# Kernel tuning notes

Hardware: AMD Instinct MI355X
Metric: run time of the kernel (lower is better)

The kernel has to match this reference:

```python
import jax, jax.numpy as jnp
import numpy as np

EPS = 1e-8
THR = 1e-6


def setup_inputs() -> dict:
    key = jax.random.key(0)
    ks = jax.random.split(key, 16)
    B, N, E, F, H, NH = 2, 8192, 131072, 128, 256, 4
    D = H // NH          # per-head width = 64
    FEAT = 2 * F + 12    # 268 = 2F + radial + dist + dot + 9 so3
    s = 0.05
    return {
        "h": jax.random.normal(ks[0], (B, N, F), jnp.float32),
        "coord": jax.random.normal(ks[1], (B, N, 3), jnp.float32),
        "edge_index": jax.random.randint(ks[2], (2, E), 0, N),
        "edge_w1": jax.random.normal(ks[3], (NH, FEAT, D), jnp.float32) * s,
        "edge_b1": jnp.zeros((NH, D), jnp.float32),
        "edge_w2": jax.random.normal(ks[4], (NH, D, D), jnp.float32) * s,
        "edge_b2": jnp.zeros((NH, D), jnp.float32),
        "ln_g": jnp.ones((H,), jnp.float32),
        "ln_b": jnp.zeros((H,), jnp.float32),
        "node_w1": jax.random.normal(ks[5], (H + F, H), jnp.float32) * s,
        "node_b1": jnp.zeros((H,), jnp.float32),
        "node_w2": jax.random.normal(ks[6], (H, F), jnp.float32) * s,
        "node_b2": jnp.zeros((F,), jnp.float32),
        "coord_w1": jax.random.normal(ks[7], (H, H), jnp.float32) * s,
        "coord_b1": jnp.zeros((H,), jnp.float32),
        "coord_w2": jax.random.normal(ks[8], (H, 1), jnp.float32) * 0.001,  # xavier gain 0.001
    }


def reference(h, coord, edge_index, edge_w1, edge_b1, edge_w2, edge_b2,
              ln_g, ln_b, node_w1, node_b1, node_w2, node_b2,
              coord_w1, coord_b1, coord_w2):
    B, N, F = h.shape
    row, col = edge_index[0], edge_index[1]
    ci, ck = coord[:, row], coord[:, col]            # (B,E,3) gathers
    coord_diff = ci - ck
    radial = jnp.sum(coord_diff * coord_diff, axis=-1, keepdims=True)
    dist = jnp.sqrt(radial)
    dot = jnp.sum(ci * ck, axis=-1, keepdims=True)
    # SO3 local frame per edge
    a = coord_diff / (dist + EPS)
    cr = jnp.cross(ci, ck)
    b = cr / (jnp.linalg.norm(cr, axis=-1, keepdims=True) + EPS)
    c = jnp.cross(a, b)
    bad = ((jnp.linalg.norm(a, axis=-1) < THR) |
           (jnp.linalg.norm(b, axis=-1) < THR) |
           (jnp.linalg.norm(c, axis=-1) < THR))
    so3 = jnp.stack([a, b, c], axis=-1)              # (B,E,3,3) columns a,b,c
    eye = jnp.broadcast_to(jnp.eye(3, dtype=so3.dtype), so3.shape)
    so3 = jnp.where(bad[..., None, None], eye, so3).reshape(B, -1, 9)
    # edge features -> multi-head edge MLPs
    feat = jnp.concatenate([h[:, row], h[:, col], radial, dist, dot, so3], axis=-1)  # (B,E,268)
    hmid = jax.nn.silu(jnp.einsum('bef,hfd->bhed', feat, edge_w1) + edge_b1[None, :, None, :])
    heads = jnp.einsum('bhed,hdk->bhek', hmid, edge_w2) + edge_b2[None, :, None, :]
    combined = jnp.moveaxis(heads, 1, 2).reshape(B, heads.shape[2], -1)  # (B,E,H)
    mu = jnp.mean(combined, axis=-1, keepdims=True)
    var = jnp.var(combined, axis=-1, keepdims=True)
    edge_feat = (combined - mu) / jnp.sqrt(var + 1e-5) * ln_g + ln_b
    # coordinate update: scatter-add weighted coord_diff
    w = jax.nn.silu(edge_feat @ coord_w1 + coord_b1) @ coord_w2   # (B,E,1)
    seg = lambda d: jax.ops.segment_sum(d, row, num_segments=N)
    coord_out = coord + jax.vmap(seg)(coord_diff * w)
    # node update: scatter-add edge features then MLP with residual
    agg = jax.vmap(seg)(edge_feat)                                # (B,N,H)
    out = jnp.concatenate([h, agg], axis=-1)
    out = jax.nn.silu(out @ node_w1 + node_b1) @ node_w2 + node_b2
    return h + out, coord_out
```

## Files before the change

### kernel.cpp

```cpp
#include <hip/hip_runtime.h>
#include <hip/hip_bf16.h>
#include <cstdint>
#include <cstddef>

#define BB 2
#define NN 8192
#define EE 131072
#define FFdim 128
#define HHdim 256
#define NHEAD 4
#define DHEAD 64
#define FEATD 268
#define K1PAD 288
#define SF 296
#define SH 264
#define TE 64
#define NT 32
#define SA 392
#define SM 264

typedef short bf16x8 __attribute__((ext_vector_type(8)));
typedef float floatx4 __attribute__((ext_vector_type(4)));

__device__ __forceinline__ float silu_f(float x) {
    return x * __fdividef(1.0f, 1.0f + __expf(-x));
}
__device__ __forceinline__ unsigned short f2bf(float x) {
    unsigned int u = __float_as_uint(x);
    unsigned int r = (u + 0x7fffu + ((u >> 16) & 1u)) >> 16;
    return (unsigned short)r;
}
__device__ __forceinline__ float bf2f(unsigned short u) {
    return __uint_as_float(((unsigned int)u) << 16);
}
__device__ __forceinline__ unsigned int pk2bf(float x, float y) {
    float2 f = { x, y };
    __hip_bfloat162 t = __float22bfloat162_rn(f);
    union { __hip_bfloat162 b; unsigned int u; } cv;
    cv.b = t;
    return cv.u;
}
__device__ __forceinline__ float rowsum16(float v) {
    v += __int_as_float(__builtin_amdgcn_update_dpp(0, __float_as_int(v), 0x128, 0xf, 0xf, true));
    v += __int_as_float(__builtin_amdgcn_update_dpp(0, __float_as_int(v), 0x124, 0xf, 0xf, true));
    v += __int_as_float(__builtin_amdgcn_update_dpp(0, __float_as_int(v), 0x122, 0xf, 0xf, true));
    v += __int_as_float(__builtin_amdgcn_update_dpp(0, __float_as_int(v), 0x121, 0xf, 0xf, true));
    return v;
}
__device__ __forceinline__ int operm(int p) { return ((p & 3) << 4) | (p >> 2); }

#define W1T_ELEMS (256 * K1PAD)
#define W2T_ELEMS (256 * 64)
#define CW1T_ELEMS (256 * 256)
#define NW1T_ELEMS (256 * 384)
#define NW2T_ELEMS (128 * 256)
#define HBF_ELEMS (BB * NN * FFdim)
#define WT_A (W1T_ELEMS)
#define WT_B (W1T_ELEMS + W2T_ELEMS)
#define WT_C (W1T_ELEMS + W2T_ELEMS + CW1T_ELEMS)
#define WT_D (WT_C + NW1T_ELEMS)
#define WT_E (WT_D + NW2T_ELEMS)
#define WT_F (WT_E + NN)
#define WT_G (WT_F + HBF_ELEMS)
__global__ void prep_weights(const float* __restrict__ w1,
                             const float* __restrict__ w2,
                             const float* __restrict__ cw1,
                             const float* __restrict__ nw1,
                             const float* __restrict__ nw2,
                             const float* __restrict__ h,
                             unsigned short* __restrict__ w1T,
                             unsigned short* __restrict__ w2T,
                             unsigned short* __restrict__ cw1T,
                             unsigned short* __restrict__ nw1T,
                             unsigned short* __restrict__ nw2T,
                             unsigned short* __restrict__ hbf,
                             int* __restrict__ counts) {
    int idx = blockIdx.x * blockDim.x + threadIdx.x;
    if (idx < WT_A) {
        int n = idx / K1PAD, k = idx % K1PAD;
        int hh = n >> 6, d = n & 63;
        float v = (k < FEATD) ? w1[((size_t)hh * FEATD + k) * DHEAD + d] : 0.f;
        w1T[idx] = f2bf(v);
    } else if (idx < WT_B) {
        int j = idx - WT_A;
        int n = j >> 6, p = j & 63;
        int hh = n >> 6, dout = n & 63;
        int din = operm(p);
        w2T[j] = f2bf(w2[(size_t)hh * 4096 + din * 64 + dout]);
    } else if (idx < WT_C) {
        int j = idx - WT_B;
        int n = j >> 8, P = j & 255;
        int ko = (P >> 6) * 64 + operm(P & 63);
        cw1T[j] = f2bf(cw1[ko * 256 + n]);
    } else if (idx < WT_D) {
        int j = idx - WT_C;
        int n = j / 384, k = j % 384;
        int ko = (k < 128) ? k : 128 + ((k - 128) >> 6) * 64 + operm(k & 63);
        nw1T[j] = f2bf(nw1[ko * 256 + n]);
    } else if (idx < WT_E) {
        int j = idx - WT_D;
        int n = j >> 8, P = j & 255;
        int ko = (P >> 6) * 64 + operm(P & 63);
        nw2T[j] = f2bf(nw2[ko * 128 + n]);
    } else if (idx < WT_F) {
        counts[idx - WT_E] = 0;
    } else if (idx < WT_G) {
        int j = idx - WT_F;
        hbf[j] = f2bf(h[j]);
    }
}

__global__ void csr_count(const int* __restrict__ eidx, int* __restrict__ counts) {
    int e = blockIdx.x * 256 + threadIdx.x;
    atomicAdd(&counts[eidx[e]], 1);
}

__global__ void csr_scan(const int* __restrict__ counts,
                         int* __restrict__ offsets,
                         int* __restrict__ cursor) {
    __shared__ int wsum[4];
    const int t = threadIdx.x;
    const int base = t * 32;
    int local[32];
#pragma unroll
    for (int q = 0; q < 8; ++q) {
        uint4 c4 = ((const uint4*)counts)[t * 8 + q];
        local[q * 4 + 0] = c4.x; local[q * 4 + 1] = c4.y;
        local[q * 4 + 2] = c4.z; local[q * 4 + 3] = c4.w;
    }
    int s = 0;
#pragma unroll
    for (int i = 0; i < 32; ++i) s += local[i];
    const int lane = t & 63, w = t >> 6;
    int v = s;
#pragma unroll
    for (int off = 1; off < 64; off <<= 1) {
        int u = __shfl_up(v, off, 64);
        if (lane >= off) v += u;
    }
    if (lane == 63) wsum[w] = v;
    __syncthreads();
    int wbase = 0;
    for (int i = 0; i < w; ++i) wbase += wsum[i];
    int run = wbase + v - s;
#pragma unroll
    for (int i = 0; i < 32; ++i) {
        offsets[base + i] = run;
        cursor[base + i] = run;
        cursor[NN + base + i] = run;
        run += local[i];
    }
    if (t == 255) offsets[NN] = run;
}

__global__ __launch_bounds__(256, 4)
void edge_kernel(const unsigned short* __restrict__ hbf,
                 const float* __restrict__ coord,
                 const int* __restrict__ eidx,
                 int* __restrict__ cursor,
                 const unsigned short* __restrict__ w1T, const float* __restrict__ b1,
                 const unsigned short* __restrict__ w2T, const float* __restrict__ b2,
                 const float* __restrict__ lng, const float* __restrict__ lnb,
                 const unsigned short* __restrict__ cw1T, const float* __restrict__ cb1,
                 const float* __restrict__ cw2,
                 unsigned short* __restrict__ efb, float4* __restrict__ wd) {
    __shared__ unsigned short bufA[TE * SF];
    __shared__ int slot_s[TE];
    __shared__ float cd_s[TE][3];
    __shared__ float lns[TE], lns2[TE];
    __shared__ float scr[TE * 4];

    const int tid = threadIdx.x;
    const int b = blockIdx.y;
    const int e0 = blockIdx.x * TE;
    const int lane = tid & 63;
    const int w = tid >> 6;
    const int lm = lane & 15;
    const int quad = lane >> 4;
    const int koff = quad * 8;

    if (tid < TE) {
        lns[tid] = 0.f; lns2[tid] = 0.f;
        const int e = e0 + tid;
        const int r = eidx[e], c = eidx[EE + e];
        slot_s[tid] = atomicAdd(&cursor[b * NN + r], 1);
        const float* pi = coord + ((size_t)b * NN + r) * 3;
        const float* pk = coord + ((size_t)b * NN + c) * 3;
        float ci0 = pi[0], ci1 = pi[1], ci2 = pi[2];
        float ck0 = pk[0], ck1 = pk[1], ck2 = pk[2];
        float dx = ci0 - ck0, dy = ci1 - ck1, dz = ci2 - ck2;
        float radial = dx * dx + dy * dy + dz * dz;
        float dist = sqrtf(radial);
        float dotv = ci0 * ck0 + ci1 * ck1 + ci2 * ck2;
        float inva = __fdividef(1.0f, dist + 1e-8f);
        float a0 = dx * inva, a1 = dy * inva, a2 = dz * inva;
        float cr0 = ci1 * ck2 - ci2 * ck1;
        float cr1 = ci2 * ck0 - ci0 * ck2;
        float cr2 = ci0 * ck1 - ci1 * ck0;
        float nb = sqrtf(cr0 * cr0 + cr1 * cr1 + cr2 * cr2);
        float invb = __fdividef(1.0f, nb + 1e-8f);
        float b0 = cr0 * invb, b1v = cr1 * invb, b2v = cr2 * invb;
        float c0 = a1 * b2v - a2 * b1v;
        float c1 = a2 * b0 - a0 * b2v;
        float c2 = a0 * b1v - a1 * b0;
        float na = sqrtf(a0 * a0 + a1 * a1 + a2 * a2);
        float nbn = sqrtf(b0 * b0 + b1v * b1v + b2v * b2v);
        float nc = sqrtf(c0 * c0 + c1 * c1 + c2 * c2);
        bool bad = (na < 1e-6f) || (nbn < 1e-6f) || (nc < 1e-6f);
        float s[12];
        s[0] = radial; s[1] = dist; s[2] = dotv;
        if (bad) {
            s[3] = 1.f; s[4] = 0.f; s[5] = 0.f;
            s[6] = 0.f; s[7] = 1.f; s[8] = 0.f;
            s[9] = 0.f; s[10] = 0.f; s[11] = 1.f;
        } else {
            s[3] = a0;  s[4] = b0;  s[5] = c0;
            s[6] = a1;  s[7] = b1v; s[8] = c1;
            s[9] = a2;  s[10] = b2v; s[11] = c2;
        }
        unsigned short* fp = &bufA[tid * SF];
#pragma unroll
        for (int q = 0; q < 12; ++q) fp[256 + q] = f2bf(s[q]);
#pragma unroll
        for (int q = FEATD; q < K1PAD; ++q) fp[q] = 0;
        cd_s[tid][0] = dx; cd_s[tid][1] = dy; cd_s[tid][2] = dz;
    }
    for (int idx = tid; idx < TE * 32; idx += 256) {
        const int e = idx >> 5, c16 = idx & 31;
        const int node = (c16 < 16) ? eidx[e0 + e] : eidx[EE + e0 + e];
        const int cc = (c16 & 15) * 8;
        uint4 v = *(const uint4*)&hbf[((size_t)b * NN + node) * FFdim + cc];
        *(uint4*)&bufA[e * SF + c16 * 8] = v;
    }
    __syncthreads();

    floatx4 acc[4][4];
#pragma unroll
    for (int i = 0; i < 4; ++i)
#pragma unroll
        for (int j = 0; j < 4; ++j)
#pragma unroll
            for (int q = 0; q < 4; ++q) acc[i][j][q] = 0.f;
#pragma unroll
    for (int ks = 0; ks < K1PAD / 32; ++ks) {
        const int kb = ks * 32 + koff;
        bf16x8 a[4], bfr[4];
#pragma unroll
        for (int rt = 0; rt < 4; ++rt)
            a[rt] = *(const bf16x8*)&bufA[(rt * 16 + lm) * SF + kb];
#pragma unroll
        for (int ct = 0; ct < 4; ++ct)
            bfr[ct] = *(const bf16x8*)&w1T[(size_t)(w * 64 + ct * 16 + lm) * K1PAD + kb];
#pragma unroll
        for (int rt = 0; rt < 4; ++rt)
#pragma unroll
            for (int ct = 0; ct < 4; ++ct)
                acc[rt][ct] = __builtin_amdgcn_mfma_f32_16x16x32_bf16(
                    a[rt], bfr[ct], acc[rt][ct], 0, 0, 0);
    }
    float bias1[4];
#pragma unroll
    for (int ct = 0; ct < 4; ++ct) bias1[ct] = b1[w * 64 + ct * 16 + lm];
    __syncthreads();
#pragma unroll
    for (int rt = 0; rt < 4; ++rt)
#pragma unroll
        for (int reg = 0; reg < 4; ++reg) {
            const int row = rt * 16 + quad * 4 + reg;
            uint2 pk;
            pk.x = pk2bf(silu_f(acc[rt][0][reg] + bias1[0]),
                         silu_f(acc[rt][1][reg] + bias1[1]));
            pk.y = pk2bf(silu_f(acc[rt][2][reg] + bias1[2]),
                         silu_f(acc[rt][3][reg] + bias1[3]));
            *(uint2*)&bufA[row * SH + w * 64 + lm * 4] = pk;
        }

    floatx4 acc2[4][4];
#pragma unroll
    for (int i = 0; i < 4; ++i)
#pragma unroll
        for (int j = 0; j < 4; ++j)
#pragma unroll
            for (int q = 0; q < 4; ++q) acc2[i][j][q] = 0.f;
#pragma unroll
    for (int ks = 0; ks < 2; ++ks) {
        const int kb = ks * 32 + koff;
        bf16x8 a[4], bfr[4];
#pragma unroll
        for (int rt = 0; rt < 4; ++rt)
            a[rt] = *(const bf16x8*)&bufA[(rt * 16 + lm) * SH + w * 64 + kb];
#pragma unroll
        for (int ct = 0; ct < 4; ++ct)
            bfr[ct] = *(const bf16x8*)&w2T[(size_t)(w * 64 + ct * 16 + lm) * 64 + kb];
#pragma unroll
        for (int rt = 0; rt < 4; ++rt)
#pragma unroll
            for (int ct = 0; ct < 4; ++ct)
                acc2[rt][ct] = __builtin_amdgcn_mfma_f32_16x16x32_bf16(
                    a[rt], bfr[ct], acc2[rt][ct], 0, 0, 0);
    }
    float bias2[4];
#pragma unroll
    for (int ct = 0; ct < 4; ++ct) bias2[ct] = b2[w * 64 + ct * 16 + lm];
#pragma unroll
    for (int rt = 0; rt < 4; ++rt)
#pragma unroll
        for (int reg = 0; reg < 4; ++reg) {
            float s = 0.f, s2 = 0.f;
#pragma unroll
            for (int ct = 0; ct < 4; ++ct) {
                float v = acc2[rt][ct][reg] + bias2[ct];
                acc2[rt][ct][reg] = v;
                s += v; s2 += v * v;
            }
            s = rowsum16(s);
            s2 = rowsum16(s2);
            if (lm == 0) {
                const int row = rt * 16 + quad * 4 + reg;
                atomicAdd(&lns[row], s);
                atomicAdd(&lns2[row], s2);
            }
        }
    __syncthreads();
    if (tid < TE) {
        float mean = lns[tid] * (1.0f / 256.0f);
        float var = lns2[tid] * (1.0f / 256.0f) - mean * mean;
        scr[tid] = mean;
        scr[TE + tid] = rsqrtf(var + 1e-5f);
    }
    __syncthreads();
    {
        float gv[4], bv[4];
#pragma unroll
        for (int ct = 0; ct < 4; ++ct) {
            const int col = w * 64 + ct * 16 + lm;
            gv[ct] = lng[col]; bv[ct] = lnb[col];
        }
#pragma unroll
        for (int rt = 0; rt < 4; ++rt)
#pragma unroll
            for (int reg = 0; reg < 4; ++reg) {
                const int row = rt * 16 + quad * 4 + reg;
                const float mu = scr[row], rs = scr[TE + row];
                uint2 pk;
                pk.x = pk2bf((acc2[rt][0][reg] - mu) * rs * gv[0] + bv[0],
                             (acc2[rt][1][reg] - mu) * rs * gv[1] + bv[1]);
                pk.y = pk2bf((acc2[rt][2][reg] - mu) * rs * gv[2] + bv[2],
                             (acc2[rt][3][reg] - mu) * rs * gv[3] + bv[3]);
                *(uint2*)&bufA[row * SH + w * 64 + lm * 4] = pk;
            }
    }
    __syncthreads();

    floatx4 acc3[4][4];
#pragma unroll
    for (int i = 0; i < 4; ++i)
#pragma unroll
        for (int j = 0; j < 4; ++j)
#pragma unroll
            for (int q = 0; q < 4; ++q) acc3[i][j][q] = 0.f;
#pragma unroll
    for (int ks = 0; ks < 8; ++ks) {
        const int kb = ks * 32 + koff;
        bf16x8 a[4], bfr[4];
#pragma unroll
        for (int rt = 0; rt < 4; ++rt)
            a[rt] = *(const bf16x8*)&bufA[(rt * 16 + lm) * SH + kb];
#pragma unroll
        for (int ct = 0; ct < 4; ++ct)
            bfr[ct] = *(const bf16x8*)&cw1T[(size_t)(w * 64 + ct * 16 + lm) * 256 + kb];
#pragma unroll
        for (int rt = 0; rt < 4; ++rt)
#pragma unroll
            for (int ct = 0; ct < 4; ++ct)
                acc3[rt][ct] = __builtin_amdgcn_mfma_f32_16x16x32_bf16(
                    a[rt], bfr[ct], acc3[rt][ct], 0, 0, 0);
    }
    {
        float cb[4], cwv[4];
#pragma unroll
        for (int ct = 0; ct < 4; ++ct) {
            const int col = w * 64 + ct * 16 + lm;
            cb[ct] = cb1[col]; cwv[ct] = cw2[col];
        }
#pragma unroll
        for (int rt = 0; rt < 4; ++rt)
#pragma unroll
            for (int reg = 0; reg < 4; ++reg) {
                float s = 0.f;
#pragma unroll
                for (int ct = 0; ct < 4; ++ct)
                    s += silu_f(acc3[rt][ct][reg] + cb[ct]) * cwv[ct];
                s = rowsum16(s);
                if (lm == 0) scr[(rt * 16 + quad * 4 + reg) * 4 + w] = s;
            }
    }
    __syncthreads();

    if (tid < TE) {
        float ww = scr[tid * 4] + scr[tid * 4 + 1] + scr[tid * 4 + 2] + scr[tid * 4 + 3];
        float4 o = { cd_s[tid][0] * ww, cd_s[tid][1] * ww, cd_s[tid][2] * ww, 0.f };
        wd[(size_t)b * EE + slot_s[tid]] = o;
    }
    for (int idx = tid; idx < TE * 32; idx += 256) {
        const int e = idx >> 5, c = idx & 31;
        uint4 v = *(const uint4*)&bufA[e * SH + c * 8];
        *(uint4*)&efb[((size_t)b * EE + slot_s[e]) * HHdim + c * 8] = v;
    }
}

__global__ __launch_bounds__(256, 4)
void node_kernel(const float* __restrict__ h,
                 const unsigned short* __restrict__ hbf,
                 const float* __restrict__ coord,
                 const unsigned short* __restrict__ efb,
                 const float4* __restrict__ wd,
                 const int* __restrict__ offsets,
                 const unsigned short* __restrict__ nw1T, const float* __restrict__ nb1,
                 const unsigned short* __restrict__ nw2T, const float* __restrict__ nb2,
                 float* __restrict__ hout, float* __restrict__ coord_out) {
    __shared__ unsigned short bufN[NT * SA];

    const int tid = threadIdx.x;
    const int b = blockIdx.y;
    const int n0 = blockIdx.x * NT;
    const int lane = tid & 63;
    const int w = tid >> 6;
    const int lm = lane & 15;
    const int quad = lane >> 4;
    const int koff = quad * 8;
    const int half = lane >> 5;
    const int cl = lane & 31;

    for (int idx = tid; idx < NT * 16; idx += 256) {
        const int r = idx >> 4, c8 = idx & 15;
        uint4 v = *(const uint4*)&hbf[((size_t)b * NN + n0 + r) * FFdim + c8 * 8];
        *(uint4*)&bufN[r * SA + c8 * 8] = v;
    }

    for (int i = 0; i < 8; ++i) {
        const int r = w * 8 + i;
        const int n = n0 + r;
        const int o0 = offsets[n], o1 = offsets[n + 1];
        float f[8];
#pragma unroll
        for (int q = 0; q < 8; ++q) f[q] = 0.f;
        const unsigned short* ebase = efb + (size_t)b * EE * HHdim + cl * 8;
        for (int j = o0 + half; j < o1; j += 2) {
            uint4 u = *(const uint4*)(ebase + (size_t)j * HHdim);
            f[0] += bf2f((unsigned short)(u.x & 0xffff));
            f[1] += bf2f((unsigned short)(u.x >> 16));
            f[2] += bf2f((unsigned short)(u.y & 0xffff));
            f[3] += bf2f((unsigned short)(u.y >> 16));
            f[4] += bf2f((unsigned short)(u.z & 0xffff));
            f[5] += bf2f((unsigned short)(u.z >> 16));
            f[6] += bf2f((unsigned short)(u.w & 0xffff));
            f[7] += bf2f((unsigned short)(u.w >> 16));
        }
#pragma unroll
        for (int q = 0; q < 8; ++q) f[q] += __shfl_xor(f[q], 32, 64);
        if (half == 0) {
            uint4 pk;
            pk.x = pk2bf(f[0], f[1]); pk.y = pk2bf(f[2], f[3]);
            pk.z = pk2bf(f[4], f[5]); pk.w = pk2bf(f[6], f[7]);
            *(uint4*)&bufN[r * SA + FFdim + cl * 8] = pk;
        }

        float sx = 0.f, sy = 0.f, sz = 0.f;
        for (int jj = o0 + lane; jj < o1; jj += 64) {
            float4 t = wd[(size_t)b * EE + jj];
            sx += t.x; sy += t.y; sz += t.z;
        }
#pragma unroll
        for (int m = 1; m < 64; m <<= 1) {
            sx += __shfl_xor(sx, m, 64);
            sy += __shfl_xor(sy, m, 64);
            sz += __shfl_xor(sz, m, 64);
        }
        if (lane < 3) {
            const size_t cb = ((size_t)b * NN + n) * 3 + lane;
            float s = (lane == 0) ? sx : (lane == 1) ? sy : sz;
            coord_out[cb] = coord[cb] + s;
        }
    }
    __syncthreads();

    floatx4 acc[2][4];
#pragma unroll
    for (int i = 0; i < 2; ++i)
#pragma unroll
        for (int j = 0; j < 4; ++j)
#pragma unroll
            for (int q = 0; q < 4; ++q) acc[i][j][q] = 0.f;
#pragma unroll
    for (int ks = 0; ks < 12; ++ks) {
        const int kb = ks * 32 + koff;
        bf16x8 a[2], bfr[4];
#pragma unroll
        for (int rt = 0; rt < 2; ++rt)
            a[rt] = *(const bf16x8*)&bufN[(rt * 16 + lm) * SA + kb];
#pragma unroll
        for (int ct = 0; ct < 4; ++ct)
            bfr[ct] = *(const bf16x8*)&nw1T[(size_t)(w * 64 + ct * 16 + lm) * 384 + kb];
#pragma unroll
        for (int rt = 0; rt < 2; ++rt)
#pragma unroll
            for (int ct = 0; ct < 4; ++ct)
                acc[rt][ct] = __builtin_amdgcn_mfma_f32_16x16x32_bf16(
                    a[rt], bfr[ct], acc[rt][ct], 0, 0, 0);
    }
    float nb1v[4];
#pragma unroll
    for (int ct = 0; ct < 4; ++ct) nb1v[ct] = nb1[w * 64 + ct * 16 + lm];
    __syncthreads();
#pragma unroll
    for (int rt = 0; rt < 2; ++rt)
#pragma unroll
        for (int reg = 0; reg < 4; ++reg) {
            const int row = rt * 16 + quad * 4 + reg;
            uint2 pk;
            pk.x = pk2bf(silu_f(acc[rt][0][reg] + nb1v[0]),
                         silu_f(acc[rt][1][reg] + nb1v[1]));
            pk.y = pk2bf(silu_f(acc[rt][2][reg] + nb1v[2]),
                         silu_f(acc[rt][3][reg] + nb1v[3]));
            *(uint2*)&bufN[row * SM + w * 64 + lm * 4] = pk;
        }
    __syncthreads();

    floatx4 accb[2][2];
#pragma unroll
    for (int i = 0; i < 2; ++i)
#pragma unroll
        for (int j = 0; j < 2; ++j)
#pragma unroll
            for (int q = 0; q < 4; ++q) accb[i][j][q] = 0.f;
#pragma unroll
    for (int ks = 0; ks < 8; ++ks) {
        const int kb = ks * 32 + koff;
        bf16x8 a[2], bfr[2];
#pragma unroll
        for (int rt = 0; rt < 2; ++rt)
            a[rt] = *(const bf16x8*)&bufN[(rt * 16 + lm) * SM + kb];
#pragma unroll
        for (int ct = 0; ct < 2; ++ct)
            bfr[ct] = *(const bf16x8*)&nw2T[(size_t)(w * 32 + ct * 16 + lm) * 256 + kb];
#pragma unroll
        for (int rt = 0; rt < 2; ++rt)
#pragma unroll
            for (int ct = 0; ct < 2; ++ct)
                accb[rt][ct] = __builtin_amdgcn_mfma_f32_16x16x32_bf16(
                    a[rt], bfr[ct], accb[rt][ct], 0, 0, 0);
    }
#pragma unroll
    for (int ct = 0; ct < 2; ++ct) {
        const int col = w * 32 + ct * 16 + lm;
        const float bias = nb2[col];
#pragma unroll
        for (int rt = 0; rt < 2; ++rt)
#pragma unroll
            for (int reg = 0; reg < 4; ++reg) {
                const int row = rt * 16 + quad * 4 + reg;
                const size_t gi = ((size_t)b * NN + n0 + row) * FFdim + col;
                hout[gi] = accb[rt][ct][reg] + bias + h[gi];
            }
    }
}

extern "C" void kernel_launch(void* const* d_in, const int* in_sizes, int n_in,
                              void* d_out, int out_size, void* d_ws, size_t ws_size,
                              hipStream_t stream) {
    const float* h     = (const float*)d_in[0];
    const float* coord = (const float*)d_in[1];
    const int*   eidx  = (const int*)d_in[2];
    const float* w1    = (const float*)d_in[3];
    const float* b1    = (const float*)d_in[4];
    const float* w2    = (const float*)d_in[5];
    const float* b2    = (const float*)d_in[6];
    const float* lng   = (const float*)d_in[7];
    const float* lnb   = (const float*)d_in[8];
    const float* nw1   = (const float*)d_in[9];
    const float* nb1   = (const float*)d_in[10];
    const float* nw2   = (const float*)d_in[11];
    const float* nb2   = (const float*)d_in[12];
    const float* cw1   = (const float*)d_in[13];
    const float* cb1   = (const float*)d_in[14];
    const float* cw2   = (const float*)d_in[15];

    float* hout = (float*)d_out;
    float* coord_out = hout + (size_t)BB * NN * FFdim;

    char* p = (char*)d_ws;
    float4* wd = (float4*)p;                   p += (size_t)BB * EE * 16;
    unsigned short* efb = (unsigned short*)p;  p += (size_t)BB * EE * HHdim * 2;
    unsigned short* hbf = (unsigned short*)p;  p += (size_t)HBF_ELEMS * 2;
    unsigned short* w1T = (unsigned short*)p;  p += (size_t)W1T_ELEMS * 2;
    unsigned short* w2T = (unsigned short*)p;  p += (size_t)W2T_ELEMS * 2;
    unsigned short* cw1T = (unsigned short*)p; p += (size_t)CW1T_ELEMS * 2;
    unsigned short* nw1T = (unsigned short*)p; p += (size_t)NW1T_ELEMS * 2;
    unsigned short* nw2T = (unsigned short*)p; p += (size_t)NW2T_ELEMS * 2;
    int* counts = (int*)p;                     p += (size_t)NN * 4;
    int* offsets = (int*)p;                    p += (size_t)(NN + 1) * 4;
    int* cursor = (int*)p;                     p += (size_t)2 * NN * 4;

    hipLaunchKernelGGL(prep_weights, dim3((WT_G + 255) / 256), dim3(256),
                       0, stream, w1, w2, cw1, nw1, nw2, h,
                       w1T, w2T, cw1T, nw1T, nw2T, hbf, counts);
    hipLaunchKernelGGL(csr_count, dim3(EE / 256), dim3(256), 0, stream, eidx, counts);
    hipLaunchKernelGGL(csr_scan, dim3(1), dim3(256), 0, stream, counts, offsets, cursor);
    hipLaunchKernelGGL(edge_kernel, dim3(EE / TE, BB), dim3(256), 0, stream,
                       hbf, coord, eidx, cursor, w1T, b1, w2T, b2, lng, lnb,
                       cw1T, cb1, cw2, efb, wd);
    hipLaunchKernelGGL(node_kernel, dim3(NN / NT, BB), dim3(256), 0, stream,
                       h, hbf, coord, efb, wd, offsets, nw1T, nb1, nw2T, nb2,
                       hout, coord_out);
}
```

Before: 350.0 us.

## Store edge features as fp8 and precompute CSR slots in a fill kernel

```diff
diff --git a/kernel.cpp b/kernel.cpp
--- a/kernel.cpp
+++ b/kernel.cpp
@@ -21,6 +21,7 @@
 
 typedef short bf16x8 __attribute__((ext_vector_type(8)));
 typedef float floatx4 __attribute__((ext_vector_type(4)));
+typedef float floatx2 __attribute__((ext_vector_type(2)));
 
 __device__ __forceinline__ float silu_f(float x) {
     return x * __fdividef(1.0f, 1.0f + __expf(-x));
@@ -147,23 +148,30 @@
     for (int i = 0; i < 32; ++i) {
         offsets[base + i] = run;
         cursor[base + i] = run;
-        cursor[NN + base + i] = run;
         run += local[i];
     }
     if (t == 255) offsets[NN] = run;
+}
+
+__global__ void csr_fill(const int* __restrict__ eidx,
+                         int* __restrict__ cursor, int* __restrict__ perm) {
+    int e = blockIdx.x * 256 + threadIdx.x;
+    int r = eidx[e];
+    int pos = atomicAdd(&cursor[r], 1);
+    perm[e] = pos;
 }
 
 __global__ __launch_bounds__(256, 4)
 void edge_kernel(const unsigned short* __restrict__ hbf,
                  const float* __restrict__ coord,
                  const int* __restrict__ eidx,
-                 int* __restrict__ cursor,
+                 const int* __restrict__ perm,
                  const unsigned short* __restrict__ w1T, const float* __restrict__ b1,
                  const unsigned short* __restrict__ w2T, const float* __restrict__ b2,
                  const float* __restrict__ lng, const float* __restrict__ lnb,
                  const unsigned short* __restrict__ cw1T, const float* __restrict__ cb1,
                  const float* __restrict__ cw2,
-                 unsigned short* __restrict__ efb, float4* __restrict__ wd) {
+                 unsigned char* __restrict__ efb, float4* __restrict__ wd) {
     __shared__ unsigned short bufA[TE * SF];
     __shared__ int slot_s[TE];
     __shared__ float cd_s[TE][3];
@@ -183,7 +191,7 @@
         lns[tid] = 0.f; lns2[tid] = 0.f;
         const int e = e0 + tid;
         const int r = eidx[e], c = eidx[EE + e];
-        slot_s[tid] = atomicAdd(&cursor[b * NN + r], 1);
+        slot_s[tid] = perm[e];
         const float* pi = coord + ((size_t)b * NN + r) * 3;
         const float* pk = coord + ((size_t)b * NN + c) * 3;
         float ci0 = pi[0], ci1 = pi[1], ci2 = pi[2];
@@ -405,7 +413,16 @@
     for (int idx = tid; idx < TE * 32; idx += 256) {
         const int e = idx >> 5, c = idx & 31;
         uint4 v = *(const uint4*)&bufA[e * SH + c * 8];
-        *(uint4*)&efb[((size_t)b * EE + slot_s[e]) * HHdim + c * 8] = v;
+        float f0 = bf2f((unsigned short)(v.x & 0xffff)), f1 = bf2f((unsigned short)(v.x >> 16));
+        float f2 = bf2f((unsigned short)(v.y & 0xffff)), f3 = bf2f((unsigned short)(v.y >> 16));
+        float f4 = bf2f((unsigned short)(v.z & 0xffff)), f5 = bf2f((unsigned short)(v.z >> 16));
+        float f6 = bf2f((unsigned short)(v.w & 0xffff)), f7 = bf2f((unsigned short)(v.w >> 16));
+        unsigned int lo = __builtin_amdgcn_cvt_pk_fp8_f32(f0, f1, 0, false);
+        lo = __builtin_amdgcn_cvt_pk_fp8_f32(f2, f3, lo, true);
+        unsigned int hi = __builtin_amdgcn_cvt_pk_fp8_f32(f4, f5, 0, false);
+        hi = __builtin_amdgcn_cvt_pk_fp8_f32(f6, f7, hi, true);
+        uint2 o = { lo, hi };
+        *(uint2*)&efb[((size_t)b * EE + slot_s[e]) * HHdim + c * 8] = o;
     }
 }
 
@@ -413,7 +430,7 @@
 void node_kernel(const float* __restrict__ h,
                  const unsigned short* __restrict__ hbf,
                  const float* __restrict__ coord,
-                 const unsigned short* __restrict__ efb,
+                 const unsigned char* __restrict__ efb,
                  const float4* __restrict__ wd,
                  const int* __restrict__ offsets,
                  const unsigned short* __restrict__ nw1T, const float* __restrict__ nb1,
@@ -445,17 +462,15 @@
         float f[8];
 #pragma unroll
         for (int q = 0; q < 8; ++q) f[q] = 0.f;
-        const unsigned short* ebase = efb + (size_t)b * EE * HHdim + cl * 8;
+        const unsigned char* ebase = efb + (size_t)b * EE * HHdim + cl * 8;
         for (int j = o0 + half; j < o1; j += 2) {
-            uint4 u = *(const uint4*)(ebase + (size_t)j * HHdim);
-            f[0] += bf2f((unsigned short)(u.x & 0xffff));
-            f[1] += bf2f((unsigned short)(u.x >> 16));
-            f[2] += bf2f((unsigned short)(u.y & 0xffff));
-            f[3] += bf2f((unsigned short)(u.y >> 16));
-            f[4] += bf2f((unsigned short)(u.z & 0xffff));
-            f[5] += bf2f((unsigned short)(u.z >> 16));
-            f[6] += bf2f((unsigned short)(u.w & 0xffff));
-            f[7] += bf2f((unsigned short)(u.w >> 16));
+            uint2 u = *(const uint2*)(ebase + (size_t)j * HHdim);
+            floatx2 p0 = __builtin_amdgcn_cvt_pk_f32_fp8(u.x, false);
+            floatx2 p1 = __builtin_amdgcn_cvt_pk_f32_fp8(u.x, true);
+            floatx2 p2 = __builtin_amdgcn_cvt_pk_f32_fp8(u.y, false);
+            floatx2 p3 = __builtin_amdgcn_cvt_pk_f32_fp8(u.y, true);
+            f[0] += p0[0]; f[1] += p0[1]; f[2] += p1[0]; f[3] += p1[1];
+            f[4] += p2[0]; f[5] += p2[1]; f[6] += p3[0]; f[7] += p3[1];
         }
 #pragma unroll
         for (int q = 0; q < 8; ++q) f[q] += __shfl_xor(f[q], 32, 64);
@@ -471,12 +486,10 @@
             float4 t = wd[(size_t)b * EE + jj];
             sx += t.x; sy += t.y; sz += t.z;
         }
-#pragma unroll
-        for (int m = 1; m < 64; m <<= 1) {
-            sx += __shfl_xor(sx, m, 64);
-            sy += __shfl_xor(sy, m, 64);
-            sz += __shfl_xor(sz, m, 64);
-        }
+        sx = rowsum16(sx); sy = rowsum16(sy); sz = rowsum16(sz);
+        sx += __shfl_xor(sx, 16, 64); sx += __shfl_xor(sx, 32, 64);
+        sy += __shfl_xor(sy, 16, 64); sy += __shfl_xor(sy, 32, 64);
+        sz += __shfl_xor(sz, 16, 64); sz += __shfl_xor(sz, 32, 64);
         if (lane < 3) {
             const size_t cb = ((size_t)b * NN + n) * 3 + lane;
             float s = (lane == 0) ? sx : (lane == 1) ? sy : sz;
@@ -591,7 +604,7 @@
 
     char* p = (char*)d_ws;
     float4* wd = (float4*)p;                   p += (size_t)BB * EE * 16;
-    unsigned short* efb = (unsigned short*)p;  p += (size_t)BB * EE * HHdim * 2;
+    unsigned char* efb = (unsigned char*)p;    p += (size_t)BB * EE * HHdim;
     unsigned short* hbf = (unsigned short*)p;  p += (size_t)HBF_ELEMS * 2;
     unsigned short* w1T = (unsigned short*)p;  p += (size_t)W1T_ELEMS * 2;
     unsigned short* w2T = (unsigned short*)p;  p += (size_t)W2T_ELEMS * 2;
@@ -600,15 +613,17 @@
     unsigned short* nw2T = (unsigned short*)p; p += (size_t)NW2T_ELEMS * 2;
     int* counts = (int*)p;                     p += (size_t)NN * 4;
     int* offsets = (int*)p;                    p += (size_t)(NN + 1) * 4;
-    int* cursor = (int*)p;                     p += (size_t)2 * NN * 4;
+    int* cursor = (int*)p;                     p += (size_t)NN * 4;
+    int* perm = (int*)p;                       p += (size_t)EE * 4;
 
     hipLaunchKernelGGL(prep_weights, dim3((WT_G + 255) / 256), dim3(256),
                        0, stream, w1, w2, cw1, nw1, nw2, h,
                        w1T, w2T, cw1T, nw1T, nw2T, hbf, counts);
     hipLaunchKernelGGL(csr_count, dim3(EE / 256), dim3(256), 0, stream, eidx, counts);
     hipLaunchKernelGGL(csr_scan, dim3(1), dim3(256), 0, stream, counts, offsets, cursor);
+    hipLaunchKernelGGL(csr_fill, dim3(EE / 256), dim3(256), 0, stream, eidx, cursor, perm);
     hipLaunchKernelGGL(edge_kernel, dim3(EE / TE, BB), dim3(256), 0, stream,
-                       hbf, coord, eidx, cursor, w1T, b1, w2T, b2, lng, lnb,
+                       hbf, coord, eidx, perm, w1T, b1, w2T, b2, lng, lnb,
                        cw1T, cb1, cw2, efb, wd);
     hipLaunchKernelGGL(node_kernel, dim3(NN / NT, BB), dim3(256), 0, stream,
                        h, hbf, coord, efb, wd, offsets, nw1T, nb1, nw2T, nb2,
```

After: 349.4 us. About the same (-0.2%).
